# Optimization experiments

Measured on AMD Instinct MI355X. Metric: run time of the kernel, lower is better.

Reference implementation:

```python
import jax, jax.numpy as jnp
import numpy as np

B, T, H, IN, OUT = 256, 1024, 512, 2, 2


def setup_inputs() -> dict:
    key = jax.random.key(0)
    ks = jax.random.split(key, 12)
    s = 1.0 / np.sqrt(H)
    return {
        "X0": jax.random.normal(ks[0], (B, OUT), jnp.float32),
        "V": jax.random.normal(ks[1], (B, T, IN), jnp.float32),
        # GRU params (torch layout: gates ordered r, z, n)
        "W_ih": jax.random.uniform(ks[2], (3 * H, IN), jnp.float32, -s, s),
        "W_hh": jax.random.uniform(ks[3], (3 * H, H), jnp.float32, -s, s),
        "b_ih": jax.random.uniform(ks[4], (3 * H,), jnp.float32, -s, s),
        "b_hh": jax.random.uniform(ks[5], (3 * H,), jnp.float32, -s, s),
        # attention MLP: Linear(OUT+IN, H//2) -> ReLU -> Linear(H//2, OUT) -> Softmax
        "Wa1": jax.random.uniform(ks[6], (H // 2, OUT + IN), jnp.float32, -s, s),
        "ba1": jax.random.uniform(ks[7], (H // 2,), jnp.float32, -s, s),
        "Wa2": jax.random.uniform(ks[8], (OUT, H // 2), jnp.float32, -s, s),
        "ba2": jax.random.uniform(ks[9], (OUT,), jnp.float32, -s, s),
        # residual layer: Linear(H, OUT)
        "Wr": jax.random.uniform(ks[10], (OUT, H), jnp.float32, -s, s),
        "br": jax.random.uniform(ks[11], (OUT,), jnp.float32, -s, s),
    }


def _forward(X0, V, W_ih, W_hh, b_ih, b_hh, Wa1, ba1, Wa2, ba2, Wr, br):
    # ---- GRU over time (batch_first input, h0 = 0) ----
    # Precompute input projections for all steps: [B, T, 3H]
    gx_all = jnp.einsum('bti,gi->btg', V, W_ih) + b_ih
    gx_tm = jnp.swapaxes(gx_all, 0, 1)  # [T, B, 3H]

    def gru_step(h, gx):
        gh = h @ W_hh.T + b_hh  # [B, 3H]
        r = jax.nn.sigmoid(gx[:, :H] + gh[:, :H])
        z = jax.nn.sigmoid(gx[:, H:2 * H] + gh[:, H:2 * H])
        n = jnp.tanh(gx[:, 2 * H:] + r * gh[:, 2 * H:])
        h_new = (1.0 - z) * n + z * h
        return h_new, h_new

    h0 = jnp.zeros((V.shape[0], H), V.dtype)
    _, h_seq = jax.lax.scan(gru_step, h0, gx_tm)  # [T, B, H]

    # residual_raw = residual_layer(h_t), precomputed for all t: [T, B, OUT]
    res_all = jnp.einsum('tbh,oh->tbo', h_seq, Wr) + br

    v_tm = jnp.swapaxes(V, 0, 1)  # [T, B, IN]; IN == OUT so slice is identity

    def corr_step(x_prev, inp):
        v_t, res_t = inp
        att_in = jnp.concatenate([x_prev, v_t[:, :OUT]], axis=-1)  # [B, OUT+IN]
        hid = jax.nn.relu(att_in @ Wa1.T + ba1)
        aw = jax.nn.softmax(hid @ Wa2.T + ba2, axis=-1)  # [B, OUT]
        x_t = x_prev + v_t[:, :OUT] + aw * res_t
        return x_t, x_t

    _, x_seq = jax.lax.scan(corr_step, X0, (v_tm, res_all))  # [T, B, OUT]
    return jnp.swapaxes(x_seq, 0, 1)  # [B, T, OUT]


def reference(X0, V, W_ih, W_hh, b_ih, b_hh, Wa1, ba1, Wa2, ba2, Wr, br):
    return _forward(X0, V, W_ih, W_hh, b_ih, b_hh, Wa1, ba1, Wa2, ba2, Wr, br)
```

## Files before the change

kernel.cpp:

```cpp
#include <hip/hip_runtime.h>


typedef short bf16x8 __attribute__((ext_vector_type(8)));
typedef float f32x4  __attribute__((ext_vector_type(4)));
typedef unsigned u32x2 __attribute__((ext_vector_type(2)));
typedef unsigned u32x4 __attribute__((ext_vector_type(4)));

__device__ __forceinline__ unsigned f2bf(float f) {
  unsigned u = __builtin_bit_cast(unsigned, f);
  return (u + 0x7fffu + ((u >> 16) & 1u)) >> 16;
}

#define KSTEP(kt, areg) \
  acc0 = __builtin_amdgcn_mfma_f32_16x16x32_bf16(areg, wf0[kt], acc0, 0, 0, 0); \
  acc1 = __builtin_amdgcn_mfma_f32_16x16x32_bf16(areg, wf1[kt], acc1, 0, 0, 0); \
  acc2 = __builtin_amdgcn_mfma_f32_16x16x32_bf16(areg, wf2[kt], acc2, 0, 0, 0);

#define PUBA(off, val) \
  asm volatile("global_atomic_swap_x2 %0, %1, off offset:" #off " sc1" \
               :: "v"(pp), "v"(val) : "memory")

__global__ void __launch_bounds__(256, 1) gru_phase1(
    const float* __restrict__ V, const float* __restrict__ W_ih,
    const float* __restrict__ W_hh, const float* __restrict__ b_ih,
    const float* __restrict__ b_hh, const float* __restrict__ Wr,
    float* __restrict__ res_part,
    char* __restrict__ hbuf)
{
  const int tid  = threadIdx.x;
  const int w    = tid >> 6;
  const int lane = tid & 63;
  const int cl   = lane & 15;
  const int hi4  = lane >> 4;
  const int g    = blockIdx.x & 15;
  const int p    = (blockIdx.x >> 4) & 7;

  __shared__ short hs[2][16][512];
  __shared__ float rscratch[4][16][2];
  char* lds = (char*)hs;

  const int c = p * 64 + w * 16 + cl;

  const float wir0 = W_ih[c * 2 + 0],          wir1 = W_ih[c * 2 + 1];
  const float wiz0 = W_ih[(512 + c) * 2 + 0],  wiz1 = W_ih[(512 + c) * 2 + 1];
  const float win0 = W_ih[(1024 + c) * 2 + 0], win1 = W_ih[(1024 + c) * 2 + 1];
  const float bsr = b_ih[c] + b_hh[c];
  const float bsz = b_ih[512 + c] + b_hh[512 + c];
  const float bin = b_ih[1024 + c];
  const float bhn = b_hh[1024 + c];
  const float wr0 = Wr[c], wr1 = Wr[512 + c];

  bf16x8 wf0[16], wf1[16], wf2[16];
  #pragma unroll
  for (int gt = 0; gt < 3; ++gt) {
    const float* src = W_hh + ((size_t)(gt * 512 + c)) * 512 + hi4 * 8;
    #pragma unroll
    for (int kt = 0; kt < 16; ++kt) {
      float4 x = *reinterpret_cast<const float4*>(src + kt * 32);
      float4 y = *reinterpret_cast<const float4*>(src + kt * 32 + 4);
      bf16x8 t;
      t[0] = (short)f2bf(x.x); t[1] = (short)f2bf(x.y);
      t[2] = (short)f2bf(x.z); t[3] = (short)f2bf(x.w);
      t[4] = (short)f2bf(y.x); t[5] = (short)f2bf(y.y);
      t[6] = (short)f2bf(y.z); t[7] = (short)f2bf(y.w);
      if (gt == 0) wf0[kt] = t; else if (gt == 1) wf1[kt] = t; else wf2[kt] = t;
    }
  }

  for (int i = tid; i < 8192; i += 256) ((unsigned*)lds)[i] = 0;
  __syncthreads();

  const int urow = tid >> 4, ucol = tid & 15;
  const unsigned roff = (unsigned)(urow * 256 + ucol * 16);

  float h[4] = {0.f, 0.f, 0.f, 0.f};

  for (int s = 0; s < 1024; ++s) {
    float2 vv[4];
    #pragma unroll
    for (int j = 0; j < 4; ++j)
      vv[j] = *reinterpret_cast<const float2*>(
          &V[((size_t)(g * 16 + hi4 * 4 + j) * 1024 + (size_t)s) * 2]);

    f32x4 acc0 = {0.f,0.f,0.f,0.f}, acc1 = {0.f,0.f,0.f,0.f}, acc2 = {0.f,0.f,0.f,0.f};
    if (s > 0) {
      const char* ab = lds + (s & 1) * 16384 + cl * 1024;
      const unsigned sw = (unsigned)((cl & 7) << 4);
      #pragma unroll
      for (int kb = 0; kb < 4; ++kb) {
        bf16x8 a0 = *(const bf16x8*)(ab + (((kb * 4 + 0) * 64 + hi4 * 16) ^ sw));
        bf16x8 a1 = *(const bf16x8*)(ab + (((kb * 4 + 1) * 64 + hi4 * 16) ^ sw));
        bf16x8 a2 = *(const bf16x8*)(ab + (((kb * 4 + 2) * 64 + hi4 * 16) ^ sw));
        bf16x8 a3 = *(const bf16x8*)(ab + (((kb * 4 + 3) * 64 + hi4 * 16) ^ sw));
        KSTEP(kb * 4 + 0, a0) KSTEP(kb * 4 + 1, a1)
        KSTEP(kb * 4 + 2, a2) KSTEP(kb * 4 + 3, a3)
      }
    }

    float hn_[4];
    #pragma unroll
    for (int j = 0; j < 4; ++j) {
      float pr = acc0[j] + bsr + wir0 * vv[j].x + wir1 * vv[j].y;
      float pz = acc1[j] + bsz + wiz0 * vv[j].x + wiz1 * vv[j].y;
      float rg = 1.f / (1.f + __expf(-pr));
      float zg = 1.f / (1.f + __expf(-pz));
      float pn = win0 * vv[j].x + win1 * vv[j].y + bin + rg * (acc2[j] + bhn);
      pn = fminf(fmaxf(pn, -30.f), 30.f);
      float e2 = __expf(2.f * pn);
      float tg = (e2 - 1.f) / (e2 + 1.f);
      hn_[j] = (1.f - zg) * tg + zg * h[j];
      h[j] = hn_[j];
    }

    unsigned pk[4];
    #pragma unroll
    for (int j = 0; j < 4; ++j) {
      float o = __shfl_xor(hn_[j], 1);
      pk[j] = f2bf(hn_[j]) | (f2bf(o) << 16);
    }

    if (!(cl & 1)) {
      char* pp = hbuf + (size_t)(s & 1) * 524288 + (size_t)(g * 8 + p) * 4096
               + (unsigned)(hi4 * 4) * 256u + (unsigned)((w * 16 + cl) >> 1) * 8u;
      u32x2 v0, v1, v2, v3;
      v0.x = pk[0]; v0.y = (unsigned)(s + 1);
      v1.x = pk[1]; v1.y = (unsigned)(s + 1);
      v2.x = pk[2]; v2.y = (unsigned)(s + 1);
      v3.x = pk[3]; v3.y = (unsigned)(s + 1);
      PUBA(0, v0); PUBA(256, v1); PUBA(512, v2); PUBA(768, v3);
    }

    if (!(cl & 1)) {
      char* wb = lds + ((s + 1) & 1) * 16384;
      const unsigned bc = (unsigned)(2 * c);
      #pragma unroll
      for (int j = 0; j < 4; ++j) {
        const unsigned row = (unsigned)(hi4 * 4 + j);
        *(unsigned*)(wb + row * 1024 + (bc ^ ((row & 7) << 4))) = pk[j];
      }
    }

    {
      float p0[4], p1[4];
      #pragma unroll
      for (int j = 0; j < 4; ++j) { p0[j] = wr0 * hn_[j]; p1[j] = wr1 * hn_[j]; }
      #pragma unroll
      for (int m = 1; m < 16; m <<= 1) {
        #pragma unroll
        for (int j = 0; j < 4; ++j) {
          p0[j] += __shfl_xor(p0[j], m);
          p1[j] += __shfl_xor(p1[j], m);
        }
      }
      if (cl == 0) {
        #pragma unroll
        for (int j = 0; j < 4; ++j) {
          rscratch[w][hi4 * 4 + j][0] = p0[j];
          rscratch[w][hi4 * 4 + j][1] = p1[j];
        }
      }
    }
    __syncthreads();

    if (tid < 16) {
      float r0 = rscratch[0][tid][0] + rscratch[1][tid][0] +
                 rscratch[2][tid][0] + rscratch[3][tid][0];
      float r1 = rscratch[0][tid][1] + rscratch[1][tid][1] +
                 rscratch[2][tid][1] + rscratch[3][tid][1];
      float2 val; val.x = r0; val.y = r1;
      *reinterpret_cast<float2*>(
          &res_part[(((size_t)s * 256 + g * 16 + tid) * 8 + p) * 2]) = val;
    }

    if (s < 1023) {
      char* wb = lds + ((s + 1) & 1) * 16384;
      const unsigned want = (unsigned)(s + 1);
      const char* sbase = hbuf + (size_t)(s & 1) * 524288 + (size_t)(g * 8) * 4096 + roff;
      u32x4 u0, u1, u2, u3, u4, u5, u6;
      unsigned pend = 0x7f;
      #define RP(r) ((p + (r) + 1) & 7)
      #define ISSUE(r, ureg) \
        if (pend & (1u << (r))) { \
          const char* src = sbase + RP(r) * 4096; \
          asm volatile("global_load_dwordx4 %0, %1, off sc1" \
                       : "=v"(ureg) : "v"(src) : "memory"); \
        }
      #define HARVEST(r, ureg) \
        if ((pend & (1u << (r))) && ureg.y == want && ureg.w == want) { \
          const unsigned bc = (unsigned)(RP(r) * 128 + ucol * 8); \
          uint2 pay; pay.x = ureg.x; pay.y = ureg.z; \
          *(uint2*)(wb + (unsigned)urow * 1024 + \
                    (bc ^ (((unsigned)urow & 7) << 4))) = pay; \
          pend &= ~(1u << (r)); \
        }
      int gd = 0;
      while (pend) {
        ISSUE(0, u0) ISSUE(1, u1) ISSUE(2, u2) ISSUE(3, u3)
        ISSUE(4, u4) ISSUE(5, u5) ISSUE(6, u6)
        asm volatile("s_waitcnt vmcnt(0)" ::: "memory");
        HARVEST(0, u0) HARVEST(1, u1) HARVEST(2, u2) HARVEST(3, u3)
        HARVEST(4, u4) HARVEST(5, u5) HARVEST(6, u6)
        if (++gd > (1 << 14)) break;
      }
      #undef RP
      #undef ISSUE
      #undef HARVEST
    }
    __syncthreads();
  }
}

__global__ void __launch_bounds__(256) corr_phase2(
    const float* __restrict__ X0,
    const float* __restrict__ V,
    const float* __restrict__ Wa1,
    const float* __restrict__ ba1,
    const float* __restrict__ Wa2,
    const float* __restrict__ ba2,
    const float* __restrict__ br,
    const float* __restrict__ res_part,
    float* __restrict__ out)
{
  const int tid = threadIdx.x;
  const int wv = tid >> 6;
  const int lane = tid & 63;
  const int b = blockIdx.x * 4 + wv;

  float w1[4][4], bb1[4], w20[4], w21[4];
  #pragma unroll
  for (int q = 0; q < 4; q++) {
    const int h = lane * 4 + q;
    #pragma unroll
    for (int c = 0; c < 4; c++) w1[q][c] = Wa1[h * 4 + c];
    bb1[q] = ba1[h];
    w20[q] = Wa2[h];
    w21[q] = Wa2[256 + h];
  }
  const float c20 = ba2[0], c21 = ba2[1];
  const float br0 = br[0], br1 = br[1];
  float x0 = X0[b * 2], x1 = X0[b * 2 + 1];

  for (int c = 0; c < 16; c++) {
    const int tl = c * 64 + lane;
    const float2 vvl = *reinterpret_cast<const float2*>(&V[(b * 1024 + tl) * 2]);
    const float4* rp = reinterpret_cast<const float4*>(
        &res_part[((size_t)tl * 256 + b) * 16]);
    float4 q0 = rp[0], q1 = rp[1], q2 = rp[2], q3 = rp[3];
    float rr0 = (q0.x + q0.z) + (q1.x + q1.z) + (q2.x + q2.z) + (q3.x + q3.z);
    float rr1 = (q0.y + q0.w) + (q1.y + q1.w) + (q2.y + q2.w) + (q3.y + q3.w);
    float sx = 0.f, sy = 0.f;
    for (int k = 0; k < 64; k++) {
      const float v0 = __shfl(vvl.x, k);
      const float v1 = __shfl(vvl.y, k);
      const float r0 = __shfl(rr0, k) + br0;
      const float r1 = __shfl(rr1, k) + br1;
      float l0 = 0.f, l1 = 0.f;
      #pragma unroll
      for (int q = 0; q < 4; q++) {
        float hq = w1[q][0] * x0 + w1[q][1] * x1 + w1[q][2] * v0 + w1[q][3] * v1 + bb1[q];
        hq = fmaxf(hq, 0.f);
        l0 += w20[q] * hq;
        l1 += w21[q] * hq;
      }
      #pragma unroll
      for (int m = 1; m < 64; m <<= 1) {
        l0 += __shfl_xor(l0, m);
        l1 += __shfl_xor(l1, m);
      }
      l0 += c20; l1 += c21;
      const float mx = fmaxf(l0, l1);
      const float e0 = __expf(l0 - mx), e1 = __expf(l1 - mx);
      const float inv = 1.f / (e0 + e1);
      x0 += v0 + (e0 * inv) * r0;
      x1 += v1 + (e1 * inv) * r1;
      if (k == lane) { sx = x0; sy = x1; }
    }
    float2 o; o.x = sx; o.y = sy;
    *reinterpret_cast<float2*>(&out[(b * 1024 + c * 64 + lane) * 2]) = o;
  }
}

extern "C" void kernel_launch(void* const* d_in, const int* in_sizes, int n_in,
                              void* d_out, int out_size, void* d_ws, size_t ws_size,
                              hipStream_t stream) {
  const float* X0   = (const float*)d_in[0];
  const float* V    = (const float*)d_in[1];
  const float* W_ih = (const float*)d_in[2];
  const float* W_hh = (const float*)d_in[3];
  const float* b_ih = (const float*)d_in[4];
  const float* b_hh = (const float*)d_in[5];
  const float* Wa1  = (const float*)d_in[6];
  const float* ba1  = (const float*)d_in[7];
  const float* Wa2  = (const float*)d_in[8];
  const float* ba2  = (const float*)d_in[9];
  const float* Wr   = (const float*)d_in[10];
  const float* br   = (const float*)d_in[11];
  float* out = (float*)d_out;

  char* ws = (char*)d_ws;
  char*  hbuf     = ws;
  float* res_part = (float*)(ws + 1024 * 1024);
  hipMemsetAsync(hbuf, 0, 1024 * 1024, stream);

  hipLaunchKernelGGL(gru_phase1, dim3(128), dim3(256), 0, stream,
                     V, W_ih, W_hh, b_ih, b_hh, Wr, res_part, hbuf);
  hipLaunchKernelGGL(corr_phase2, dim3(64), dim3(256), 0, stream,
                     X0, V, Wa1, ba1, Wa2, ba2, br, res_part, out);
}
```

Baseline: 3.389 ms.

## Fuse correction recurrence into GRU kernel, computing residual from shared hidden state

Removes the separate correction kernel and the res_part round trip. The GRU kernel now runs the correction step inside its time loop: two waves per block each handle one batch row, computing the residual projection from the full bf16 hidden state in LDS plus the attention MLP. The per-step reduction __syncthreads is dropped, and the other two waves sleep briefly before polling for peer blocks. This adds serial work to the GRU critical path each step, and the residual now uses bf16-rounded hidden values.

New measurement: 3.190 ms. -5.9%, faster.

```diff
diff --git a/kernel.cpp b/kernel.cpp
--- a/kernel.cpp
+++ b/kernel.cpp
@@ -10,6 +10,10 @@
   unsigned u = __builtin_bit_cast(unsigned, f);
   return (u + 0x7fffu + ((u >> 16) & 1u)) >> 16;
 }
+__device__ __forceinline__ float bf2f(unsigned short u) {
+  unsigned v = (unsigned)u << 16;
+  return __builtin_bit_cast(float, v);
+}
 
 #define KSTEP(kt, areg) \
   acc0 = __builtin_amdgcn_mfma_f32_16x16x32_bf16(areg, wf0[kt], acc0, 0, 0, 0); \
@@ -20,11 +24,14 @@
   asm volatile("global_atomic_swap_x2 %0, %1, off offset:" #off " sc1" \
                :: "v"(pp), "v"(val) : "memory")
 
-__global__ void __launch_bounds__(256, 1) gru_phase1(
+__global__ void __launch_bounds__(256, 1) gru_fused(
     const float* __restrict__ V, const float* __restrict__ W_ih,
     const float* __restrict__ W_hh, const float* __restrict__ b_ih,
     const float* __restrict__ b_hh, const float* __restrict__ Wr,
-    float* __restrict__ res_part,
+    const float* __restrict__ Wa1, const float* __restrict__ ba1,
+    const float* __restrict__ Wa2, const float* __restrict__ ba2v,
+    const float* __restrict__ brv, const float* __restrict__ X0,
+    float* __restrict__ out,
     char* __restrict__ hbuf)
 {
   const int tid  = threadIdx.x;
@@ -36,7 +43,10 @@
   const int p    = (blockIdx.x >> 4) & 7;
 
   __shared__ short hs[2][16][512];
-  __shared__ float rscratch[4][16][2];
+  __shared__ float wrl[2][512];
+  __shared__ float wa1l[1024];
+  __shared__ float ba1l[256];
+  __shared__ float wa2l[2][256];
   char* lds = (char*)hs;
 
   const int c = p * 64 + w * 16 + cl;
@@ -48,7 +58,9 @@
   const float bsz = b_ih[512 + c] + b_hh[512 + c];
   const float bin = b_ih[1024 + c];
   const float bhn = b_hh[1024 + c];
-  const float wr0 = Wr[c], wr1 = Wr[512 + c];
+
+  const float ba2_0 = ba2v[0], ba2_1 = ba2v[1];
+  const float br0 = brv[0], br1 = brv[1];
 
   bf16x8 wf0[16], wf1[16], wf2[16];
   #pragma unroll
@@ -68,12 +80,64 @@
   }
 
   for (int i = tid; i < 8192; i += 256) ((unsigned*)lds)[i] = 0;
+  for (int i = tid; i < 512; i += 256) { wrl[0][i] = Wr[i]; wrl[1][i] = Wr[512 + i]; }
+  for (int i = tid; i < 1024; i += 256) wa1l[i] = Wa1[i];
+  if (tid < 256) { ba1l[tid] = ba1[tid]; wa2l[0][tid] = Wa2[tid]; wa2l[1][tid] = Wa2[256 + tid]; }
   __syncthreads();
 
   const int urow = tid >> 4, ucol = tid & 15;
   const unsigned roff = (unsigned)(urow * 256 + ucol * 16);
 
   float h[4] = {0.f, 0.f, 0.f, 0.f};
+
+  float x0 = 0.f, x1 = 0.f;
+  if (w < 2) {
+    const int gr = g * 16 + 2 * p + w;
+    x0 = X0[gr * 2 + 0];
+    x1 = X0[gr * 2 + 1];
+  }
+
+  auto corr = [&](int sl) {
+    const int row = 2 * p + w;
+    const int gr  = g * 16 + row;
+    const int t   = sl - 1;
+    const char* hb = lds + (sl & 1) * 16384 + row * 1024;
+    const unsigned off = ((unsigned)(lane * 16)) ^ (((unsigned)row & 7) << 4);
+    bf16x8 hv = *(const bf16x8*)(hb + off);
+    float r0 = 0.f, r1 = 0.f;
+    #pragma unroll
+    for (int k2 = 0; k2 < 8; ++k2) {
+      float hf = bf2f((unsigned short)hv[k2]);
+      r0 += wrl[0][lane * 8 + k2] * hf;
+      r1 += wrl[1][lane * 8 + k2] * hf;
+    }
+    const float2 vt = *reinterpret_cast<const float2*>(&V[((size_t)gr * 1024 + t) * 2]);
+    float l0 = 0.f, l1 = 0.f;
+    #pragma unroll
+    for (int q = 0; q < 4; ++q) {
+      const int hh = lane * 4 + q;
+      float4 wa = *reinterpret_cast<const float4*>(&wa1l[hh * 4]);
+      float hq = wa.x * x0 + wa.y * x1 + wa.z * vt.x + wa.w * vt.y + ba1l[hh];
+      hq = fmaxf(hq, 0.f);
+      l0 += wa2l[0][hh] * hq;
+      l1 += wa2l[1][hh] * hq;
+    }
+    #pragma unroll
+    for (int m = 1; m < 64; m <<= 1) {
+      r0 += __shfl_xor(r0, m); r1 += __shfl_xor(r1, m);
+      l0 += __shfl_xor(l0, m); l1 += __shfl_xor(l1, m);
+    }
+    l0 += ba2_0; l1 += ba2_1;
+    const float mx = fmaxf(l0, l1);
+    const float e0 = __expf(l0 - mx), e1 = __expf(l1 - mx);
+    const float inv = 1.f / (e0 + e1);
+    x0 += vt.x + (e0 * inv) * (r0 + br0);
+    x1 += vt.y + (e1 * inv) * (r1 + br1);
+    if (lane == 0) {
+      float2 o; o.x = x0; o.y = x1;
+      *reinterpret_cast<float2*>(&out[((size_t)gr * 1024 + t) * 2]) = o;
+    }
+  };
 
   for (int s = 0; s < 1024; ++s) {
     float2 vv[4];
@@ -140,44 +204,15 @@
       }
     }
 
+    if (s > 0 && w < 2) corr(s);
+
     {
-      float p0[4], p1[4];
-      #pragma unroll
-      for (int j = 0; j < 4; ++j) { p0[j] = wr0 * hn_[j]; p1[j] = wr1 * hn_[j]; }
-      #pragma unroll
-      for (int m = 1; m < 16; m <<= 1) {
-        #pragma unroll
-        for (int j = 0; j < 4; ++j) {
-          p0[j] += __shfl_xor(p0[j], m);
-          p1[j] += __shfl_xor(p1[j], m);
-        }
-      }
-      if (cl == 0) {
-        #pragma unroll
-        for (int j = 0; j < 4; ++j) {
-          rscratch[w][hi4 * 4 + j][0] = p0[j];
-          rscratch[w][hi4 * 4 + j][1] = p1[j];
-        }
-      }
-    }
-    __syncthreads();
-
-    if (tid < 16) {
-      float r0 = rscratch[0][tid][0] + rscratch[1][tid][0] +
-                 rscratch[2][tid][0] + rscratch[3][tid][0];
-      float r1 = rscratch[0][tid][1] + rscratch[1][tid][1] +
-                 rscratch[2][tid][1] + rscratch[3][tid][1];
-      float2 val; val.x = r0; val.y = r1;
-      *reinterpret_cast<float2*>(
-          &res_part[(((size_t)s * 256 + g * 16 + tid) * 8 + p) * 2]) = val;
-    }
-
-    if (s < 1023) {
       char* wb = lds + ((s + 1) & 1) * 16384;
       const unsigned want = (unsigned)(s + 1);
       const char* sbase = hbuf + (size_t)(s & 1) * 524288 + (size_t)(g * 8) * 4096 + roff;
       u32x4 u0, u1, u2, u3, u4, u5, u6;
       unsigned pend = 0x7f;
+      if (w >= 2) __builtin_amdgcn_s_sleep(8);
       #define RP(r) ((p + (r) + 1) & 7)
       #define ISSUE(r, ureg) \
         if (pend & (1u << (r))) { \
@@ -208,76 +243,8 @@
     }
     __syncthreads();
   }
-}
-
-__global__ void __launch_bounds__(256) corr_phase2(
-    const float* __restrict__ X0,
-    const float* __restrict__ V,
-    const float* __restrict__ Wa1,
-    const float* __restrict__ ba1,
-    const float* __restrict__ Wa2,
-    const float* __restrict__ ba2,
-    const float* __restrict__ br,
-    const float* __restrict__ res_part,
-    float* __restrict__ out)
-{
-  const int tid = threadIdx.x;
-  const int wv = tid >> 6;
-  const int lane = tid & 63;
-  const int b = blockIdx.x * 4 + wv;
-
-  float w1[4][4], bb1[4], w20[4], w21[4];
-  #pragma unroll
-  for (int q = 0; q < 4; q++) {
-    const int h = lane * 4 + q;
-    #pragma unroll
-    for (int c = 0; c < 4; c++) w1[q][c] = Wa1[h * 4 + c];
-    bb1[q] = ba1[h];
-    w20[q] = Wa2[h];
-    w21[q] = Wa2[256 + h];
-  }
-  const float c20 = ba2[0], c21 = ba2[1];
-  const float br0 = br[0], br1 = br[1];
-  float x0 = X0[b * 2], x1 = X0[b * 2 + 1];
-
-  for (int c = 0; c < 16; c++) {
-    const int tl = c * 64 + lane;
-    const float2 vvl = *reinterpret_cast<const float2*>(&V[(b * 1024 + tl) * 2]);
-    const float4* rp = reinterpret_cast<const float4*>(
-        &res_part[((size_t)tl * 256 + b) * 16]);
-    float4 q0 = rp[0], q1 = rp[1], q2 = rp[2], q3 = rp[3];
-    float rr0 = (q0.x + q0.z) + (q1.x + q1.z) + (q2.x + q2.z) + (q3.x + q3.z);
-    float rr1 = (q0.y + q0.w) + (q1.y + q1.w) + (q2.y + q2.w) + (q3.y + q3.w);
-    float sx = 0.f, sy = 0.f;
-    for (int k = 0; k < 64; k++) {
-      const float v0 = __shfl(vvl.x, k);
-      const float v1 = __shfl(vvl.y, k);
-      const float r0 = __shfl(rr0, k) + br0;
-      const float r1 = __shfl(rr1, k) + br1;
-      float l0 = 0.f, l1 = 0.f;
-      #pragma unroll
-      for (int q = 0; q < 4; q++) {
-        float hq = w1[q][0] * x0 + w1[q][1] * x1 + w1[q][2] * v0 + w1[q][3] * v1 + bb1[q];
-        hq = fmaxf(hq, 0.f);
-        l0 += w20[q] * hq;
-        l1 += w21[q] * hq;
-      }
-      #pragma unroll
-      for (int m = 1; m < 64; m <<= 1) {
-        l0 += __shfl_xor(l0, m);
-        l1 += __shfl_xor(l1, m);
-      }
-      l0 += c20; l1 += c21;
-      const float mx = fmaxf(l0, l1);
-      const float e0 = __expf(l0 - mx), e1 = __expf(l1 - mx);
-      const float inv = 1.f / (e0 + e1);
-      x0 += v0 + (e0 * inv) * r0;
-      x1 += v1 + (e1 * inv) * r1;
-      if (k == lane) { sx = x0; sy = x1; }
-    }
-    float2 o; o.x = sx; o.y = sy;
-    *reinterpret_cast<float2*>(&out[(b * 1024 + c * 64 + lane) * 2]) = o;
-  }
+
+  if (w < 2) corr(1024);
 }
 
 extern "C" void kernel_launch(void* const* d_in, const int* in_sizes, int n_in,
@@ -297,13 +264,10 @@
   const float* br   = (const float*)d_in[11];
   float* out = (float*)d_out;
 
-  char* ws = (char*)d_ws;
-  char*  hbuf     = ws;
-  float* res_part = (float*)(ws + 1024 * 1024);
+  char* hbuf = (char*)d_ws;
   hipMemsetAsync(hbuf, 0, 1024 * 1024, stream);
 
-  hipLaunchKernelGGL(gru_phase1, dim3(128), dim3(256), 0, stream,
-                     V, W_ih, W_hh, b_ih, b_hh, Wr, res_part, hbuf);
-  hipLaunchKernelGGL(corr_phase2, dim3(64), dim3(256), 0, stream,
-                     X0, V, Wa1, ba1, Wa2, ba2, br, res_part, out);
-}
+  hipLaunchKernelGGL(gru_fused, dim3(128), dim3(256), 0, stream,
+                     V, W_ih, W_hh, b_ih, b_hh, Wr,
+                     Wa1, ba1, Wa2, ba2, br, X0, out, hbuf);
+}
```
